# Kernel tuning notes

Hardware: AMD Instinct MI355X
Metric: run time of the kernel (lower is better)

The kernel has to match this reference:

```python
import jax, jax.numpy as jnp
import numpy as np

N, K, D = 8192, 64, 256


def setup_inputs() -> dict:
    key = jax.random.key(0)
    k1, k2, k3, k4 = jax.random.split(key, 4)
    x = jax.random.normal(k1, (N, D), dtype=jnp.float32)
    mu = jax.random.normal(k2, (K, D), dtype=jnp.float32)
    # Build SPD, well-conditioned covariances: A A^T / D + I
    A = jax.random.normal(k3, (K, D, D), dtype=jnp.float32)
    var = jnp.einsum('kde,kfe->kdf', A, A) / D + jnp.eye(D, dtype=jnp.float32)
    pi = jax.nn.softmax(jax.random.normal(k4, (K,), dtype=jnp.float32))
    return {"x": x, "mu": mu, "var": var, "pi": pi}


def _weighted_log_prob(x, mu, var, pi):
    d = x.shape[-1]
    precision = jnp.linalg.inv(var)                    # (K, D, D)
    # log|precision| via cholesky, nan_to_num(0) as in the torch code
    L = jnp.linalg.cholesky(precision)                 # (K, D, D)
    log_det = 2.0 * jnp.sum(jnp.log(jnp.diagonal(L, axis1=-2, axis2=-1)), axis=-1)
    log_det = jnp.nan_to_num(log_det, nan=0.0)         # (K,)
    xm = x[:, None, :] - mu[None, :, :]                # (N, K, D)
    # Mahalanobis quadratic form: (x-mu)^T P (x-mu), vectorized over clusters
    quad = jnp.einsum('nkd,kde,nke->nk', xm, precision, xm)  # (N, K)
    log_2pi = d * jnp.log(2.0 * jnp.pi)
    log_prob = -0.5 * (log_2pi - log_det[None, :] + quad)     # (N, K)
    return log_prob + jnp.log(pi)[None, :]


def reference(x, mu, var, pi):
    # Eval-mode GMM forward: hard cluster assignment (argmax over weighted log prob)
    weighted = _weighted_log_prob(x, mu, var, pi)
    return jnp.argmax(weighted, axis=1)
```

## Files before the change

kernel.cpp:

```cpp
#include <hip/hip_runtime.h>
#include <math.h>

#define D 256
#define KC 64
#define NPTS 8192
#define TRI ((D*(D+1))/2)

#define WSZ 33920
#define FR_PER_CL 72
#define SH_PER_CL (FR_PER_CL*512)
#define SLAB_SH ((size_t)(3*SH_PER_CL))

typedef __attribute__((ext_vector_type(8))) short short8;
typedef __attribute__((ext_vector_type(4))) float f32x4;

__device__ __forceinline__ int wb(int r) {
  return ((r*(r+1)/2 + 3) & ~3) + (r << 2);
}
__device__ __forceinline__ unsigned short f2bf(float f) {
  unsigned u = __float_as_uint(f);
  u = (u + 0x7fffu + ((u >> 16) & 1u)) >> 16;
  return (unsigned short)u;
}
__device__ __forceinline__ float bf2f(unsigned short s) { return __uint_as_float(((unsigned)s) << 16); }
__device__ __forceinline__ float rdlane(float v, int l) {
  return __uint_as_float(__builtin_amdgcn_readlane(__float_as_uint(v), l));
}
__device__ __forceinline__ int frag_off(int I) { int a = I >> 1; return (I & 1) ? (a+1)*(a+1) : a*(a+1); }

__global__ __launch_bounds__(512, 1) void gmm_chol(
    const float* __restrict__ var, unsigned short* __restrict__ planes)
{
  __shared__ float W[WSZ];
  __shared__ float Tbuf[32*36];

  const int k = blockIdx.x, tid = threadIdx.x;
  const int lane = tid & 63, wid = tid >> 6;
  const float* A = var + (size_t)k*D*D;

  for (int idx = tid; idx < TRI; idx += 512) {
    int i = (int)((sqrtf(8.0f*(float)idx + 1.0f) - 1.0f)*0.5f);
    while ((i+1)*(i+2)/2 <= idx) ++i;
    while (i*(i+1)/2 > idx) --i;
    const int p = idx - i*(i+1)/2;
    W[wb(i) + p] = A[i*D + p];
  }
  __syncthreads();

#pragma unroll 1
  for (int jb = 0; jb < 8; ++jb) {
    const int c0 = jb*32, c1 = c0 + 32, m = 256 - c1;

    if (wid == 0 && lane < 32) {
      const int rbase = wb(c0 + lane) + c0;
      float Arow[32];
#pragma unroll
      for (int p = 0; p < 32; ++p) Arow[p] = W[rbase + p];

      float mydinv = 0.0f;
#pragma unroll
      for (int j = 0; j < 32; ++j) {
        const float dj = sqrtf(rdlane(Arow[j], j));
        const float dinv = 1.0f / dj;
        const float c = Arow[j] * dinv;
        Arow[j] = (lane == j) ? dj : c;
        mydinv = (lane == j) ? dinv : mydinv;
#pragma unroll
        for (int p = j + 1; p < 32; ++p) {
          const float cp = rdlane(c, p);
          Arow[p] -= c * cp;
        }
      }

#pragma unroll
      for (int p = 0; p < 32; ++p) {
        const float lp = (lane > p) ? Arow[p] : 0.0f;
#pragma unroll
        for (int j = 0; j < p; ++j) {
          const float fin = (0.0f - Arow[j]) * mydinv;
          Arow[j] = (lane == p) ? fin : Arow[j];
        }
        Arow[p] = (lane == p) ? mydinv : Arow[p];
#pragma unroll
        for (int j = 0; j < p; ++j) {
          const float gpj = rdlane(Arow[j], p);
          Arow[j] += lp * gpj;
        }
        const float gpp = rdlane(Arow[p], p);
        Arow[p] = (lane > p) ? (lp * gpp) : Arow[p];
      }

#pragma unroll
      for (int j = 0; j < 32; ++j) {
        if (j <= lane) W[rbase + j] = Arow[j];
        Tbuf[lane*36 + j] = (j <= lane) ? Arow[j] : 0.0f;
      }
    }
    __syncthreads();

    {
      const int m2 = 2*m;
      const int r = tid >> 1, jh = tid & 1;
      const int rb = wb(c1 + r) + c0;
      float row[32];
      if (tid < m2) {
#pragma unroll
        for (int p4 = 0; p4 < 8; ++p4) {
          const float4 v = *reinterpret_cast<const float4*>(&W[rb + p4*4]);
          row[p4*4+0] = v.x; row[p4*4+1] = v.y; row[p4*4+2] = v.z; row[p4*4+3] = v.w;
        }
      }
      __syncthreads();
      if (tid < m2) {
        const int j0 = jh*16;
#pragma unroll 1
        for (int j = j0; j < j0 + 16; ++j) {
          const float* up = &Tbuf[j*36];
          float s0 = 0.f, s1 = 0.f, s2 = 0.f, s3 = 0.f;
#pragma unroll
          for (int p4 = 0; p4 < 8; ++p4) {
            const float4 u = *reinterpret_cast<const float4*>(&up[p4*4]);
            s0 += row[p4*4+0]*u.x; s1 += row[p4*4+1]*u.y;
            s2 += row[p4*4+2]*u.z; s3 += row[p4*4+3]*u.w;
          }
          W[rb + j] = (s0 + s1) + (s2 + s3);
        }
      }
    }
    __syncthreads();

    if (m > 0) {
      const int nt = m >> 2, ntri = nt*(nt+1)/2;
      for (int tau = tid; tau < ntri; tau += 512) {
        int ti = (int)((sqrtf(8.0f*(float)tau + 1.0f) - 1.0f)*0.5f);
        while ((ti+1)*(ti+2)/2 <= tau) ++ti;
        while (ti*(ti+1)/2 > tau) --ti;
        const int tl = tau - ti*(ti+1)/2;
        const int i0 = c1 + ti*4, l0 = c1 + tl*4;
        const int ib[4] = {wb(i0)+c0, wb(i0+1)+c0, wb(i0+2)+c0, wb(i0+3)+c0};
        const int lb[4] = {wb(l0)+c0, wb(l0+1)+c0, wb(l0+2)+c0, wb(l0+3)+c0};
        float acc[4][4];
#pragma unroll
        for (int a = 0; a < 4; ++a)
#pragma unroll
          for (int b = 0; b < 4; ++b) acc[a][b] = 0.0f;
#pragma unroll
        for (int p4 = 0; p4 < 8; ++p4) {
          float4 av[4], bv[4];
#pragma unroll
          for (int a = 0; a < 4; ++a) av[a] = *reinterpret_cast<const float4*>(&W[ib[a] + p4*4]);
#pragma unroll
          for (int b = 0; b < 4; ++b) bv[b] = *reinterpret_cast<const float4*>(&W[lb[b] + p4*4]);
#pragma unroll
          for (int a = 0; a < 4; ++a)
#pragma unroll
            for (int b = 0; b < 4; ++b)
              acc[a][b] += av[a].x*bv[b].x + av[a].y*bv[b].y + av[a].z*bv[b].z + av[a].w*bv[b].w;
        }
#pragma unroll
        for (int a = 0; a < 4; ++a)
#pragma unroll
          for (int b = 0; b < 4; ++b) {
            const int rr = i0 + a, cc = l0 + b;
            if (cc <= rr) W[wb(rr) + cc] -= acc[a][b];
          }
      }
    }
    __syncthreads();
  }

  float* Wgk = (float*)(planes + (size_t)k*SLAB_SH);
  for (int idx = tid; idx < WSZ; idx += 512) Wgk[idx] = W[idx];
}

__global__ __launch_bounds__(512, 1) void gmm_inv3(unsigned short* __restrict__ planes)
{
  __shared__ float W[WSZ];
  __shared__ float Tbuf[32*36];

  const int b = blockIdx.x, k = b/3, part = b - 3*(b/3);
  const int tid = threadIdx.x;
  float* Wgk = (float*)(planes + (size_t)k*SLAB_SH);
  for (int idx = tid; idx < WSZ; idx += 512) W[idx] = Wgk[idx];
  __syncthreads();

  const unsigned cols = (part == 0) ? 0x21u : (part == 1) ? 0x12u : 0xCCu;
  const int i0 = tid >> 4;
  const int j0g = (tid & 15) * 2;

#pragma unroll 1
  for (int J = 0; J < 8; ++J) {
    if (!(cols & (1u << J))) continue;
#pragma unroll 1
    for (int I = J + 1; I < 8; ++I) {
      float acc0 = 0.f, acc1 = 0.f;
      for (int K = J; K < I; ++K) {
        const int abase = wb(32*I + i0) + 32*K;
        const int brow = 32*K, bcol = 32*J + j0g;
        const bool dK = (K == J);
#pragma unroll
        for (int p4 = 0; p4 < 8; ++p4) {
          const float4 av = *reinterpret_cast<const float4*>(&W[abase + p4*4]);
          const float a4[4] = {av.x, av.y, av.z, av.w};
#pragma unroll
          for (int pp = 0; pp < 4; ++pp) {
            const int p = p4*4 + pp;
            const float2 bv = *reinterpret_cast<const float2*>(&W[wb(brow + p) + bcol]);
            float b0 = bv.x, b1 = bv.y;
            if (dK) { if (j0g > p) b0 = 0.f; if (j0g + 1 > p) b1 = 0.f; }
            acc0 += a4[pp]*b0; acc1 += a4[pp]*b1;
          }
        }
      }
      Tbuf[i0*36 + j0g] = acc0;
      Tbuf[i0*36 + j0g + 1] = acc1;
      __syncthreads();

      float g0 = 0.f, g1 = 0.f;
      const int ubase = wb(32*I + i0) + 32*I;
#pragma unroll
      for (int p4 = 0; p4 < 8; ++p4) {
        const float4 uv = *reinterpret_cast<const float4*>(&W[ubase + p4*4]);
        const float u4[4] = {uv.x, uv.y, uv.z, uv.w};
#pragma unroll
        for (int pp = 0; pp < 4; ++pp) {
          const int p = p4*4 + pp;
          const float u = (p <= i0) ? u4[pp] : 0.f;
          const float2 tv = *reinterpret_cast<const float2*>(&Tbuf[p*36 + j0g]);
          g0 += u*tv.x; g1 += u*tv.y;
        }
      }
      __syncthreads();
      {
        float2 wv; wv.x = -g0; wv.y = -g1;
        *reinterpret_cast<float2*>(&W[wb(32*I + i0) + 32*J + j0g]) = wv;
      }
      __syncthreads();
    }
  }

  for (int J = 0; J < 8; ++J) {
    if (!(cols & (1u << J))) continue;
    const int r0 = 32*(J + 1);
    const int nel = (256 - r0) * 32;
    for (int e = tid; e < nel; e += 512) {
      const int r = r0 + (e >> 5), c = 32*J + (e & 31);
      Wgk[wb(r) + c] = W[wb(r) + c];
    }
  }
}

__global__ __launch_bounds__(256, 1) void gmm_pack(
    unsigned short* __restrict__ planes, const float* __restrict__ mu,
    const float* __restrict__ pi, float* __restrict__ tvec,
    float* __restrict__ bias)
{
  __shared__ float W[WSZ];
  __shared__ float colbuf[D];
  __shared__ float red[256];
  const int k = blockIdx.x, tid = threadIdx.x;
  const float* Wgk = (const float*)(planes + (size_t)k*SLAB_SH);
  for (int idx = tid; idx < WSZ; idx += 256) W[idx] = Wgk[idx];
  colbuf[tid] = mu[k*D + tid];
  __syncthreads();

  {
    const int rb4 = wb(tid);
    float s = 0.0f;
    for (int p = 0; p <= tid; ++p) s += W[rb4 + p]*colbuf[p];
    tvec[k*D + tid] = s;
    red[tid] = s*s;
  }
  __syncthreads();
  for (int st = 128; st > 0; st >>= 1) { if (tid < st) red[tid] += red[tid+st]; __syncthreads(); }
  const float t2 = red[0];
  __syncthreads();
  red[tid] = logf(W[wb(tid) + tid]);
  __syncthreads();
  for (int st = 128; st > 0; st >>= 1) { if (tid < st) red[tid] += red[tid+st]; __syncthreads(); }
  if (tid == 0) bias[k] = logf(pi[k]) + red[0] - 0.5f*t2;
  __syncthreads();

  unsigned short* slab = planes + (size_t)k*SLAB_SH;
  for (int e = tid; e < SH_PER_CL; e += 256) {
    const int f = e >> 9, wrd = e & 511, l = wrd >> 3, j = wrd & 7;
    const int I = (f>=1)+(f>=2)+(f>=4)+(f>=6)+(f>=9)+(f>=12)+(f>=16)+(f>=20)
                +(f>=25)+(f>=30)+(f>=36)+(f>=42)+(f>=49)+(f>=56)+(f>=64);
    const int kc = f - frag_off(I);
    const int li = l & 15, hh = l >> 4;
    const int p = kc*32 + hh*8 + j, i2 = I*16 + li;
    const float g = (p <= i2) ? W[wb(i2) + p] : 0.0f;
    const unsigned short hb = f2bf(g); const float hf = bf2f(hb);
    const float r1 = g - hf;
    const unsigned short lb = f2bf(r1); const float lf = bf2f(lb);
    const unsigned short rb = f2bf(r1 - lf);
    slab[e] = hb;
    slab[SH_PER_CL + e] = lb;
    slab[2*SH_PER_CL + e] = rb;
  }
}

__global__ __launch_bounds__(512, 1) void gmm_score_mfma(
    const float* __restrict__ x, const unsigned short* __restrict__ planes,
    const float* __restrict__ tvec, const float* __restrict__ bias,
    float* __restrict__ partq)
{
  __shared__ uint4 shb[9216];
  const int tid = threadIdx.x, lane = tid & 63, w = tid >> 6;
  const int li = lane & 15, h = lane >> 4;
  const int kq = blockIdx.x & 7, ntile = blockIdx.x >> 3;
  const int n0 = ntile*256 + w*32;

  short8 ah[2][8], al[2][8];
#pragma unroll
  for (int s = 0; s < 2; ++s) {
    const float* xr = x + (size_t)(n0 + s*16 + li)*D;
#pragma unroll
    for (int kc = 0; kc < 8; ++kc) {
      const float4 v0 = *reinterpret_cast<const float4*>(xr + kc*32 + h*8);
      const float4 v1 = *reinterpret_cast<const float4*>(xr + kc*32 + h*8 + 4);
      const float xv[8] = {v0.x, v0.y, v0.z, v0.w, v1.x, v1.y, v1.z, v1.w};
#pragma unroll
      for (int j = 0; j < 8; ++j) {
        const unsigned short hb = f2bf(xv[j]);
        ah[s][kc][j] = (short)hb;
        al[s][kc][j] = (short)f2bf(xv[j] - bf2f(hb));
      }
    }
  }

  float best0[4], sec0[4], best1[4], sec1[4];
  int bk0[4], bk1[4];
#pragma unroll
  for (int j = 0; j < 4; ++j) {
    best0[j] = -3.0e38f; sec0[j] = -3.0e38f; bk0[j] = 0;
    best1[j] = -3.0e38f; sec1[j] = -3.0e38f; bk1[j] = 0;
  }

  const unsigned short* shs = reinterpret_cast<const unsigned short*>(shb);

#pragma unroll 1
  for (int kk = 0; kk < 8; ++kk) {
    const int k = kq*8 + kk;
    __syncthreads();
    {
      const uint4* g4 = reinterpret_cast<const uint4*>(planes + (size_t)k*SLAB_SH);
#pragma unroll
      for (int it = 0; it < 18; ++it)
        shb[it*512 + tid] = g4[it*512 + tid];
    }
    __syncthreads();

    const float* tk = tvec + k*D;
    float p0[4] = {0.f,0.f,0.f,0.f}, p1[4] = {0.f,0.f,0.f,0.f};
#pragma unroll
    for (int I = 0; I < 16; ++I) {
      const int fb = frag_off(I);
      const int kcnt = (I + 2) >> 1;
      f32x4 a0A = {0.f,0.f,0.f,0.f}, a0B = {0.f,0.f,0.f,0.f}, a0C = {0.f,0.f,0.f,0.f};
      f32x4 a1A = {0.f,0.f,0.f,0.f}, a1B = {0.f,0.f,0.f,0.f}, a1C = {0.f,0.f,0.f,0.f};
#pragma unroll
      for (int kc = 0; kc < kcnt; ++kc) {
        const int fo = (fb + kc)*512 + lane*8;
        const short8 bh = *reinterpret_cast<const short8*>(shs + fo);
        const short8 bl = *reinterpret_cast<const short8*>(shs + 36864 + fo);
        a0A = __builtin_amdgcn_mfma_f32_16x16x32_bf16(ah[0][kc], bh, a0A, 0, 0, 0);
        a1A = __builtin_amdgcn_mfma_f32_16x16x32_bf16(ah[1][kc], bh, a1A, 0, 0, 0);
        a0B = __builtin_amdgcn_mfma_f32_16x16x32_bf16(al[0][kc], bh, a0B, 0, 0, 0);
        a1B = __builtin_amdgcn_mfma_f32_16x16x32_bf16(al[1][kc], bh, a1B, 0, 0, 0);
        a0C = __builtin_amdgcn_mfma_f32_16x16x32_bf16(ah[0][kc], bl, a0C, 0, 0, 0);
        a1C = __builtin_amdgcn_mfma_f32_16x16x32_bf16(ah[1][kc], bl, a1C, 0, 0, 0);
      }
      const float t = tk[I*16 + li];
#pragma unroll
      for (int j = 0; j < 4; ++j) {
        float y = a0A[j] + (a0B[j] + a0C[j]); p0[j] += y*(t - 0.5f*y);
        y = a1A[j] + (a1B[j] + a1C[j]);       p1[j] += y*(t - 0.5f*y);
      }
    }
#pragma unroll
    for (int mloc = 1; mloc < 16; mloc <<= 1) {
#pragma unroll
      for (int j = 0; j < 4; ++j) {
        p0[j] += __shfl_xor(p0[j], mloc, 64);
        p1[j] += __shfl_xor(p1[j], mloc, 64);
      }
    }
    const float bs = bias[k];
#pragma unroll
    for (int j = 0; j < 4; ++j) {
      const float s0v = bs + p0[j];
      if (s0v > best0[j]) { sec0[j] = best0[j]; best0[j] = s0v; bk0[j] = k; }
      else if (s0v > sec0[j]) sec0[j] = s0v;
      const float s1v = bs + p1[j];
      if (s1v > best1[j]) { sec1[j] = best1[j]; best1[j] = s1v; bk1[j] = k; }
      else if (s1v > sec1[j]) sec1[j] = s1v;
    }
  }

  if (li == 0) {
#pragma unroll
    for (int j = 0; j < 4; ++j) {
      const size_t r0 = ((size_t)kq*NPTS + n0 + h*4 + j)*3;
      partq[r0] = best0[j]; partq[r0+1] = __int_as_float(bk0[j]); partq[r0+2] = sec0[j];
      const size_t r1 = ((size_t)kq*NPTS + n0 + 16 + h*4 + j)*3;
      partq[r1] = best1[j]; partq[r1+1] = __int_as_float(bk1[j]); partq[r1+2] = sec1[j];
    }
  }
}

__global__ __launch_bounds__(256) void gmm_merge(
    const float* __restrict__ partq, int* __restrict__ out,
    int* __restrict__ flaglist, int* __restrict__ flagcnt)
{
  const int n = blockIdx.x*256 + threadIdx.x;
  float b = -3.0e38f, s2 = -3.0e38f; int bk = 0;
#pragma unroll
  for (int q = 0; q < 8; ++q) {
    const size_t o = ((size_t)q*NPTS + n)*3;
    const float bq = partq[o];
    const int kq_ = __float_as_int(partq[o+1]);
    const float sq = partq[o+2];
    if (bq > b) { s2 = fmaxf(b, sq); b = bq; bk = kq_; }
    else        { s2 = fmaxf(s2, bq); }
  }
  out[n] = bk;
  if (b - s2 < 0.25f) {
    const int idx = atomicAdd(flagcnt, 1);
    flaglist[idx] = n;
  }
}

__global__ __launch_bounds__(256, 1) void gmm_escore(
    const float* __restrict__ x, const unsigned short* __restrict__ planes,
    const float* __restrict__ tvec, const float* __restrict__ bias,
    const int* __restrict__ flaglist, const int* __restrict__ flagcnt,
    float* __restrict__ escore)
{
  const int bid = blockIdx.x;
  const int k = bid & 63, gs = bid >> 6;
  const int tid = threadIdx.x, lane = tid & 63, w = tid >> 6;
  const int li = lane & 15, h = lane >> 4;
  const int cnt = *flagcnt;
  if (cnt == 0) return;

  const unsigned short* bhB = planes + (size_t)k*SLAB_SH;
  const unsigned short* blB = bhB + SH_PER_CL;
  const unsigned short* brB = bhB + 2*SH_PER_CL;
  const float* tk = tvec + k*D;
  const float bs = bias[k];

#pragma unroll 1
  for (int g = gs*4 + w; g*16 < cnt; g += 12) {
    const int slot = g*16 + li;
    const int row = (slot < cnt) ? flaglist[slot] : 0;

    short8 ah[8], al[8], ar[8];
    const float* xr = x + (size_t)row*D;
#pragma unroll
    for (int kc = 0; kc < 8; ++kc) {
      const float4 v0 = *reinterpret_cast<const float4*>(xr + kc*32 + h*8);
      const float4 v1 = *reinterpret_cast<const float4*>(xr + kc*32 + h*8 + 4);
      const float xv[8] = {v0.x, v0.y, v0.z, v0.w, v1.x, v1.y, v1.z, v1.w};
#pragma unroll
      for (int j = 0; j < 8; ++j) {
        const unsigned short hb = f2bf(xv[j]); const float hf = bf2f(hb);
        const float r1 = xv[j] - hf;
        const unsigned short lb = f2bf(r1); const float lf = bf2f(lb);
        ah[kc][j] = (short)hb; al[kc][j] = (short)lb; ar[kc][j] = (short)f2bf(r1 - lf);
      }
    }

    float p[4] = {0.f,0.f,0.f,0.f};
#pragma unroll
    for (int I = 0; I < 16; ++I) {
      const int fb = frag_off(I);
      const int kcnt = (I + 2) >> 1;
      f32x4 accA = {0.f,0.f,0.f,0.f}, accB = {0.f,0.f,0.f,0.f};
#pragma unroll
      for (int kc = 0; kc < kcnt; ++kc) {
        const int fo = (fb + kc)*512 + lane*8;
        const short8 bh = *reinterpret_cast<const short8*>(bhB + fo);
        const short8 bl = *reinterpret_cast<const short8*>(blB + fo);
        const short8 br = *reinterpret_cast<const short8*>(brB + fo);
        accA = __builtin_amdgcn_mfma_f32_16x16x32_bf16(ah[kc], bh, accA, 0, 0, 0);
        accB = __builtin_amdgcn_mfma_f32_16x16x32_bf16(al[kc], bh, accB, 0, 0, 0);
        accB = __builtin_amdgcn_mfma_f32_16x16x32_bf16(ar[kc], bh, accB, 0, 0, 0);
        accB = __builtin_amdgcn_mfma_f32_16x16x32_bf16(ah[kc], bl, accB, 0, 0, 0);
        accB = __builtin_amdgcn_mfma_f32_16x16x32_bf16(al[kc], bl, accB, 0, 0, 0);
        accB = __builtin_amdgcn_mfma_f32_16x16x32_bf16(ah[kc], br, accB, 0, 0, 0);
      }
      const float t = tk[I*16 + li];
#pragma unroll
      for (int j = 0; j < 4; ++j) {
        const float y = accA[j] + accB[j];
        p[j] += y*(t - 0.5f*y);
      }
    }
#pragma unroll
    for (int mloc = 1; mloc < 16; mloc <<= 1) {
#pragma unroll
      for (int j = 0; j < 4; ++j) p[j] += __shfl_xor(p[j], mloc, 64);
    }
    if (li == 0) {
#pragma unroll
      for (int j = 0; j < 4; ++j) {
        const int slot2 = g*16 + h*4 + j;
        if (slot2 < cnt) escore[(size_t)k*NPTS + slot2] = bs + p[j];
      }
    }
  }
}

__global__ __launch_bounds__(256) void gmm_emerge(
    const float* __restrict__ escore, const int* __restrict__ flaglist,
    const int* __restrict__ flagcnt, int* __restrict__ out)
{
  const int cnt = *flagcnt;
  const int s = blockIdx.x*256 + threadIdx.x;
  if (s >= cnt) return;
  float b = escore[s]; int bk = 0;
#pragma unroll 1
  for (int k = 1; k < KC; ++k) {
    const float v = escore[(size_t)k*NPTS + s];
    if (v > b) { b = v; bk = k; }
  }
  out[flaglist[s]] = bk;
}

extern "C" void kernel_launch(void* const* d_in, const int* in_sizes, int n_in,
                              void* d_out, int out_size, void* d_ws, size_t ws_size,
                              hipStream_t stream)
{
  const float* x   = (const float*)d_in[0];
  const float* mu  = (const float*)d_in[1];
  const float* var = (const float*)d_in[2];
  const float* pi  = (const float*)d_in[3];

  char* ws = (char*)d_ws;
  unsigned short* planes = (unsigned short*)ws;
  float* tvec = (float*)(ws + KC*SLAB_SH*sizeof(unsigned short));
  float* bias = tvec + KC*D;
  int* flaglist = (int*)(bias + 256);
  int* flagcnt = flaglist + NPTS;
  float* partq = (float*)(flagcnt + 64);
  float* escore = partq;
  int* out = (int*)d_out;

  gmm_chol<<<KC, 512, 0, stream>>>(var, planes);
  gmm_inv3<<<3*KC, 512, 0, stream>>>(planes);
  gmm_pack<<<KC, 256, 0, stream>>>(planes, mu, pi, tvec, bias);
  gmm_score_mfma<<<256, 512, 0, stream>>>(x, planes, tvec, bias, partq);
  hipMemsetAsync(flagcnt, 0, sizeof(int), stream);
  gmm_merge<<<NPTS/256, 256, 0, stream>>>(partq, out, flaglist, flagcnt);
  gmm_escore<<<3*KC, 256, 0, stream>>>(x, planes, tvec, bias, flaglist, flagcnt, escore);
  gmm_emerge<<<NPTS/256, 256, 0, stream>>>(escore, flaglist, flagcnt, out);
}
```

Baseline: 733.8 us.

## Split blocked Cholesky into per-panel kernels across many more blocks

```diff
diff --git a/kernel.cpp b/kernel.cpp
--- a/kernel.cpp
+++ b/kernel.cpp
@@ -10,6 +10,7 @@
 #define FR_PER_CL 72
 #define SH_PER_CL (FR_PER_CL*512)
 #define SLAB_SH ((size_t)(3*SH_PER_CL))
+#define UPITCH 36
 
 typedef __attribute__((ext_vector_type(8))) short short8;
 typedef __attribute__((ext_vector_type(4))) float f32x4;
@@ -28,149 +29,161 @@
 }
 __device__ __forceinline__ int frag_off(int I) { int a = I >> 1; return (I & 1) ? (a+1)*(a+1) : a*(a+1); }
 
-__global__ __launch_bounds__(512, 1) void gmm_chol(
+__global__ __launch_bounds__(256, 1) void gmm_init(
     const float* __restrict__ var, unsigned short* __restrict__ planes)
 {
-  __shared__ float W[WSZ];
-  __shared__ float Tbuf[32*36];
-
   const int k = blockIdx.x, tid = threadIdx.x;
-  const int lane = tid & 63, wid = tid >> 6;
   const float* A = var + (size_t)k*D*D;
-
-  for (int idx = tid; idx < TRI; idx += 512) {
+  float* Wg = (float*)(planes + (size_t)k*SLAB_SH);
+  for (int idx = tid; idx < TRI; idx += 256) {
     int i = (int)((sqrtf(8.0f*(float)idx + 1.0f) - 1.0f)*0.5f);
     while ((i+1)*(i+2)/2 <= idx) ++i;
     while (i*(i+1)/2 > idx) --i;
     const int p = idx - i*(i+1)/2;
-    W[wb(i) + p] = A[i*D + p];
-  }
-  __syncthreads();
-
+    Wg[wb(i) + p] = A[i*D + p];
+  }
+}
+
+__global__ __launch_bounds__(64, 1) void gmm_diag(
+    unsigned short* __restrict__ planes, float* __restrict__ Ug, int jb)
+{
+  const int k = blockIdx.x, lane = threadIdx.x & 63;
+  float* Wg = (float*)(planes + (size_t)k*SLAB_SH);
+  const int c0 = jb*32;
+
+  if (lane < 32) {
+    const int rbase = wb(c0 + lane) + c0;
+    float Arow[32];
+#pragma unroll
+    for (int p4 = 0; p4 < 8; ++p4) {
+      const float4 v = *reinterpret_cast<const float4*>(&Wg[rbase + p4*4]);
+      Arow[p4*4+0] = v.x; Arow[p4*4+1] = v.y; Arow[p4*4+2] = v.z; Arow[p4*4+3] = v.w;
+    }
+
+    float mydinv = 0.0f;
+#pragma unroll
+    for (int j = 0; j < 32; ++j) {
+      const float dj = sqrtf(rdlane(Arow[j], j));
+      const float dinv = 1.0f / dj;
+      const float c = Arow[j] * dinv;
+      Arow[j] = (lane == j) ? dj : c;
+      mydinv = (lane == j) ? dinv : mydinv;
+#pragma unroll
+      for (int p = j + 1; p < 32; ++p) {
+        const float cp = rdlane(c, p);
+        Arow[p] -= c * cp;
+      }
+    }
+
+#pragma unroll
+    for (int p = 0; p < 32; ++p) {
+      const float lp = (lane > p) ? Arow[p] : 0.0f;
+#pragma unroll
+      for (int j = 0; j < p; ++j) {
+        const float fin = (0.0f - Arow[j]) * mydinv;
+        Arow[j] = (lane == p) ? fin : Arow[j];
+      }
+      Arow[p] = (lane == p) ? mydinv : Arow[p];
+#pragma unroll
+      for (int j = 0; j < p; ++j) {
+        const float gpj = rdlane(Arow[j], p);
+        Arow[j] += lp * gpj;
+      }
+      const float gpp = rdlane(Arow[p], p);
+      Arow[p] = (lane > p) ? (lp * gpp) : Arow[p];
+    }
+
+    float* Uk = Ug + (size_t)k*32*UPITCH;
+#pragma unroll
+    for (int j = 0; j < 32; ++j) {
+      if (j <= lane) Wg[rbase + j] = Arow[j];
+      Uk[lane*UPITCH + j] = (j <= lane) ? Arow[j] : 0.0f;
+    }
+  }
+}
+
+__global__ __launch_bounds__(512, 1) void gmm_trsm(
+    unsigned short* __restrict__ planes, const float* __restrict__ Ug, int jb)
+{
+  __shared__ float Ush[32*UPITCH];
+  const int bid = blockIdx.x, k = bid >> 1, half = bid & 1;
+  const int tid = threadIdx.x;
+  float* Wg = (float*)(planes + (size_t)k*SLAB_SH);
+  const int c0 = jb*32, c1 = c0 + 32, m = 256 - c1;
+
+  for (int i = tid; i < 32*UPITCH; i += 512) Ush[i] = Ug[(size_t)k*32*UPITCH + i];
+
+  const int idx = half*512 + tid, m2 = 2*m;
+  const int r = idx >> 1, jh = idx & 1;
+  const int rb = wb(c1 + r) + c0;
+  float row[32];
+  if (idx < m2) {
+#pragma unroll
+    for (int p4 = 0; p4 < 8; ++p4) {
+      const float4 v = *reinterpret_cast<const float4*>(&Wg[rb + p4*4]);
+      row[p4*4+0] = v.x; row[p4*4+1] = v.y; row[p4*4+2] = v.z; row[p4*4+3] = v.w;
+    }
+  }
+  __syncthreads();
+  if (idx < m2) {
+    const int j0 = jh*16;
 #pragma unroll 1
-  for (int jb = 0; jb < 8; ++jb) {
-    const int c0 = jb*32, c1 = c0 + 32, m = 256 - c1;
-
-    if (wid == 0 && lane < 32) {
-      const int rbase = wb(c0 + lane) + c0;
-      float Arow[32];
-#pragma unroll
-      for (int p = 0; p < 32; ++p) Arow[p] = W[rbase + p];
-
-      float mydinv = 0.0f;
-#pragma unroll
-      for (int j = 0; j < 32; ++j) {
-        const float dj = sqrtf(rdlane(Arow[j], j));
-        const float dinv = 1.0f / dj;
-        const float c = Arow[j] * dinv;
-        Arow[j] = (lane == j) ? dj : c;
-        mydinv = (lane == j) ? dinv : mydinv;
-#pragma unroll
-        for (int p = j + 1; p < 32; ++p) {
-          const float cp = rdlane(c, p);
-          Arow[p] -= c * cp;
-        }
-      }
-
-#pragma unroll
-      for (int p = 0; p < 32; ++p) {
-        const float lp = (lane > p) ? Arow[p] : 0.0f;
-#pragma unroll
-        for (int j = 0; j < p; ++j) {
-          const float fin = (0.0f - Arow[j]) * mydinv;
-          Arow[j] = (lane == p) ? fin : Arow[j];
-        }
-        Arow[p] = (lane == p) ? mydinv : Arow[p];
-#pragma unroll
-        for (int j = 0; j < p; ++j) {
-          const float gpj = rdlane(Arow[j], p);
-          Arow[j] += lp * gpj;
-        }
-        const float gpp = rdlane(Arow[p], p);
-        Arow[p] = (lane > p) ? (lp * gpp) : Arow[p];
-      }
-
-#pragma unroll
-      for (int j = 0; j < 32; ++j) {
-        if (j <= lane) W[rbase + j] = Arow[j];
-        Tbuf[lane*36 + j] = (j <= lane) ? Arow[j] : 0.0f;
-      }
-    }
-    __syncthreads();
-
-    {
-      const int m2 = 2*m;
-      const int r = tid >> 1, jh = tid & 1;
-      const int rb = wb(c1 + r) + c0;
-      float row[32];
-      if (tid < m2) {
-#pragma unroll
-        for (int p4 = 0; p4 < 8; ++p4) {
-          const float4 v = *reinterpret_cast<const float4*>(&W[rb + p4*4]);
-          row[p4*4+0] = v.x; row[p4*4+1] = v.y; row[p4*4+2] = v.z; row[p4*4+3] = v.w;
-        }
-      }
-      __syncthreads();
-      if (tid < m2) {
-        const int j0 = jh*16;
-#pragma unroll 1
-        for (int j = j0; j < j0 + 16; ++j) {
-          const float* up = &Tbuf[j*36];
-          float s0 = 0.f, s1 = 0.f, s2 = 0.f, s3 = 0.f;
-#pragma unroll
-          for (int p4 = 0; p4 < 8; ++p4) {
-            const float4 u = *reinterpret_cast<const float4*>(&up[p4*4]);
-            s0 += row[p4*4+0]*u.x; s1 += row[p4*4+1]*u.y;
-            s2 += row[p4*4+2]*u.z; s3 += row[p4*4+3]*u.w;
-          }
-          W[rb + j] = (s0 + s1) + (s2 + s3);
-        }
-      }
-    }
-    __syncthreads();
-
-    if (m > 0) {
-      const int nt = m >> 2, ntri = nt*(nt+1)/2;
-      for (int tau = tid; tau < ntri; tau += 512) {
-        int ti = (int)((sqrtf(8.0f*(float)tau + 1.0f) - 1.0f)*0.5f);
-        while ((ti+1)*(ti+2)/2 <= tau) ++ti;
-        while (ti*(ti+1)/2 > tau) --ti;
-        const int tl = tau - ti*(ti+1)/2;
-        const int i0 = c1 + ti*4, l0 = c1 + tl*4;
-        const int ib[4] = {wb(i0)+c0, wb(i0+1)+c0, wb(i0+2)+c0, wb(i0+3)+c0};
-        const int lb[4] = {wb(l0)+c0, wb(l0+1)+c0, wb(l0+2)+c0, wb(l0+3)+c0};
-        float acc[4][4];
-#pragma unroll
-        for (int a = 0; a < 4; ++a)
-#pragma unroll
-          for (int b = 0; b < 4; ++b) acc[a][b] = 0.0f;
-#pragma unroll
-        for (int p4 = 0; p4 < 8; ++p4) {
-          float4 av[4], bv[4];
-#pragma unroll
-          for (int a = 0; a < 4; ++a) av[a] = *reinterpret_cast<const float4*>(&W[ib[a] + p4*4]);
-#pragma unroll
-          for (int b = 0; b < 4; ++b) bv[b] = *reinterpret_cast<const float4*>(&W[lb[b] + p4*4]);
-#pragma unroll
-          for (int a = 0; a < 4; ++a)
-#pragma unroll
-            for (int b = 0; b < 4; ++b)
-              acc[a][b] += av[a].x*bv[b].x + av[a].y*bv[b].y + av[a].z*bv[b].z + av[a].w*bv[b].w;
-        }
-#pragma unroll
-        for (int a = 0; a < 4; ++a)
-#pragma unroll
-          for (int b = 0; b < 4; ++b) {
-            const int rr = i0 + a, cc = l0 + b;
-            if (cc <= rr) W[wb(rr) + cc] -= acc[a][b];
-          }
-      }
-    }
-    __syncthreads();
-  }
-
-  float* Wgk = (float*)(planes + (size_t)k*SLAB_SH);
-  for (int idx = tid; idx < WSZ; idx += 512) Wgk[idx] = W[idx];
+    for (int j = j0; j < j0 + 16; ++j) {
+      const float* up = &Ush[j*UPITCH];
+      float s0 = 0.f, s1 = 0.f, s2 = 0.f, s3 = 0.f;
+#pragma unroll
+      for (int p4 = 0; p4 < 8; ++p4) {
+        const float4 u = *reinterpret_cast<const float4*>(&up[p4*4]);
+        s0 += row[p4*4+0]*u.x; s1 += row[p4*4+1]*u.y;
+        s2 += row[p4*4+2]*u.z; s3 += row[p4*4+3]*u.w;
+      }
+      Wg[rb + j] = (s0 + s1) + (s2 + s3);
+    }
+  }
+}
+
+__global__ __launch_bounds__(256, 1) void gmm_syrk(
+    unsigned short* __restrict__ planes, int jb)
+{
+  const int bid = blockIdx.x, k = bid >> 3, s = bid & 7;
+  float* Wg = (float*)(planes + (size_t)k*SLAB_SH);
+  const int c0 = jb*32, c1 = c0 + 32, m = 256 - c1;
+  const int nt = m >> 2, ntri = nt*(nt+1)/2;
+  const int tau = s*256 + threadIdx.x;
+  if (tau >= ntri) return;
+
+  int ti = (int)((sqrtf(8.0f*(float)tau + 1.0f) - 1.0f)*0.5f);
+  while ((ti+1)*(ti+2)/2 <= tau) ++ti;
+  while (ti*(ti+1)/2 > tau) --ti;
+  const int tl = tau - ti*(ti+1)/2;
+  const int i0 = c1 + ti*4, l0 = c1 + tl*4;
+  const int ib[4] = {wb(i0)+c0, wb(i0+1)+c0, wb(i0+2)+c0, wb(i0+3)+c0};
+  const int lb[4] = {wb(l0)+c0, wb(l0+1)+c0, wb(l0+2)+c0, wb(l0+3)+c0};
+  float acc[4][4];
+#pragma unroll
+  for (int a = 0; a < 4; ++a)
+#pragma unroll
+    for (int b = 0; b < 4; ++b) acc[a][b] = 0.0f;
+#pragma unroll
+  for (int p4 = 0; p4 < 8; ++p4) {
+    float4 av[4], bv[4];
+#pragma unroll
+    for (int a = 0; a < 4; ++a) av[a] = *reinterpret_cast<const float4*>(&Wg[ib[a] + p4*4]);
+#pragma unroll
+    for (int b = 0; b < 4; ++b) bv[b] = *reinterpret_cast<const float4*>(&Wg[lb[b] + p4*4]);
+#pragma unroll
+    for (int a = 0; a < 4; ++a)
+#pragma unroll
+      for (int b = 0; b < 4; ++b)
+        acc[a][b] += av[a].x*bv[b].x + av[a].y*bv[b].y + av[a].z*bv[b].z + av[a].w*bv[b].w;
+  }
+#pragma unroll
+  for (int a = 0; a < 4; ++a)
+#pragma unroll
+    for (int b = 0; b < 4; ++b) {
+      const int rr = i0 + a, cc = l0 + b;
+      if (cc <= rr) Wg[wb(rr) + cc] -= acc[a][b];
+    }
 }
 
 __global__ __launch_bounds__(512, 1) void gmm_inv3(unsigned short* __restrict__ planes)
@@ -545,9 +558,17 @@
   int* flagcnt = flaglist + NPTS;
   float* partq = (float*)(flagcnt + 64);
   float* escore = partq;
+  float* Ug = partq + (size_t)KC*NPTS;
   int* out = (int*)d_out;
 
-  gmm_chol<<<KC, 512, 0, stream>>>(var, planes);
+  gmm_init<<<KC, 256, 0, stream>>>(var, planes);
+  for (int jb = 0; jb < 8; ++jb) {
+    gmm_diag<<<KC, 64, 0, stream>>>(planes, Ug, jb);
+    if (jb < 7) {
+      gmm_trsm<<<2*KC, 512, 0, stream>>>(planes, Ug, jb);
+      gmm_syrk<<<8*KC, 256, 0, stream>>>(planes, jb);
+    }
+  }
   gmm_inv3<<<3*KC, 512, 0, stream>>>(planes);
   gmm_pack<<<KC, 256, 0, stream>>>(planes, mu, pi, tvec, bias);
   gmm_score_mfma<<<256, 512, 0, stream>>>(x, planes, tvec, bias, partq);
```

New measurement: 781.3 us. +6.5%, slower.
